# Performance work log

Measured on AMD Instinct MI355X. Metric: run time of the kernel, lower is better.

Reference implementation:

```python
import jax, jax.numpy as jnp
import numpy as np

E, T, H, I = 8, 1024, 2048, 5632  # experts, tokens/expert, hidden, intermediate


def setup_inputs() -> dict:
    key = jax.random.key(0)
    k1, k2, k3 = jax.random.split(key, 3)
    permuted_hidden_states = jax.random.normal(k1, (E * T, H), dtype=jnp.float32)
    # per-expert weights; linear is x @ W with W[in, out] (same math as nn.Linear with W^T)
    w1 = jax.random.normal(k2, (E, H, 2 * I), dtype=jnp.float32) * 0.02
    w2 = jax.random.normal(k3, (E, I, H), dtype=jnp.float32) * 0.02
    tokens_per_expert = jnp.full((E,), T, dtype=jnp.int32)
    return {
        "permuted_hidden_states": permuted_hidden_states,
        "w1": w1,
        "w2": w2,
        "tokens_per_expert": tokens_per_expert,
    }


def reference(permuted_hidden_states, w1, w2, tokens_per_expert):
    # Tokens are contiguously segmented per expert; with equal counts (static T)
    # the per-expert loop becomes one batched (grouped) GEMM.
    x = permuted_hidden_states.reshape(E, T, H)
    fc1 = jnp.einsum('eth,ehf->etf', x, w1)          # [E, T, 2I]
    a, b = jnp.split(fc1, 2, axis=-1)                # GLU: chunk last dim
    inter = jax.nn.silu(a) * b                       # [E, T, I]
    out = jnp.einsum('eti,eih->eth', inter, w2)      # [E, T, H]
    return out.reshape(E * T, H)
```

## Files before the change

kernel.cpp:

```cpp
#include <hip/hip_runtime.h>
#include <hip/hip_bf16.h>


#define EXPERTS 8
#define TOK     1024
#define HID     2048
#define INTER   5632
#define I2      (2 * INTER)

typedef __bf16 bf16x8 __attribute__((ext_vector_type(8)));
typedef float  f32x4  __attribute__((ext_vector_type(4)));

__device__ __forceinline__ unsigned short f2bf(float f) {
    union { float f; unsigned u; } v; v.f = f;
    unsigned r = v.u + 0x7FFFu + ((v.u >> 16) & 1u);
    return (unsigned short)(r >> 16);
}

__device__ __forceinline__ void gload_lds16(const void* g, void* l) {
    __builtin_amdgcn_global_load_lds(
        (const __attribute__((address_space(1))) void*)g,
        (__attribute__((address_space(3))) void*)l, 16, 0, 0);
}

__device__ __forceinline__ bf16x8 ldfrag(const unsigned short* S, int R, int kb) {
    int off = R * 64 + (kb ^ ((R & 7) << 3));
    return *reinterpret_cast<const bf16x8*>(S + off);
}


__global__ __launch_bounds__(256) void k_cvt_x(const float* __restrict__ X,
                                               unsigned short* __restrict__ Xb) {
    size_t base = ((size_t)blockIdx.x * 256 + threadIdx.x) * 8;
    int row = (int)(base >> 11);
    int k   = (int)(base & (HID - 1));
    int kp  = k ^ ((row & 7) << 3);
    float4 v0 = *reinterpret_cast<const float4*>(X + base);
    float4 v1 = *reinterpret_cast<const float4*>(X + base + 4);
    uint4 o;
    o.x = (unsigned)f2bf(v0.x) | ((unsigned)f2bf(v0.y) << 16);
    o.y = (unsigned)f2bf(v0.z) | ((unsigned)f2bf(v0.w) << 16);
    o.z = (unsigned)f2bf(v1.x) | ((unsigned)f2bf(v1.y) << 16);
    o.w = (unsigned)f2bf(v1.z) | ((unsigned)f2bf(v1.w) << 16);
    *reinterpret_cast<uint4*>(Xb + (size_t)row * HID + kp) = o;
}

__global__ __launch_bounds__(256) void k_cvt_w1(const float* __restrict__ W1,
                                                unsigned short* __restrict__ W1T) {
    __shared__ unsigned short lds[64][72];
    const int bid = blockIdx.x;
    const int hb = bid % (HID / 64);
    const int pb = (bid / (HID / 64)) % (I2 / 64);
    const int e  = bid / ((HID / 64) * (I2 / 64));
    const int h0 = hb * 64, p0 = pb * 64, n0 = p0 >> 1;
    const float* w1e = W1 + (size_t)e * HID * I2;
    const int t = threadIdx.x;
#pragma unroll
    for (int it = 0; it < 16; ++it) {
        int lin   = it * 256 + t;
        int n_off = lin & 31;
        int c     = (lin >> 5) & 1;
        int h_off = lin >> 6;
        float v = w1e[(size_t)(h0 + h_off) * I2 + c * INTER + n0 + n_off];
        lds[2 * n_off + c][h_off] = f2bf(v);
    }
    __syncthreads();
    unsigned short* o = W1T + (size_t)e * I2 * HID;
#pragma unroll
    for (int it = 0; it < 4; ++it) {
        int lin = it * 256 + t;
        int r   = lin >> 4;
        int co  = (lin & 15) * 4;
        int cop = co ^ ((r & 7) << 3);
        ushort4 v = *reinterpret_cast<ushort4*>(&lds[r][co]);
        *reinterpret_cast<ushort4*>(o + (size_t)(p0 + r) * HID + h0 + cop) = v;
    }
}

__global__ __launch_bounds__(256) void k_cvt_w2(const float* __restrict__ W2,
                                                unsigned short* __restrict__ W2T) {
    __shared__ unsigned short lds[64][72];
    const int bid = blockIdx.x;
    const int ib = bid % (INTER / 64);
    const int hb = (bid / (INTER / 64)) % (HID / 64);
    const int e  = bid / ((INTER / 64) * (HID / 64));
    const int i0 = ib * 64, h0 = hb * 64;
    const float* w2e = W2 + (size_t)e * INTER * HID;
    const int t = threadIdx.x;
#pragma unroll
    for (int it = 0; it < 16; ++it) {
        int lin   = it * 256 + t;
        int h_off = lin & 63;
        int i_off = lin >> 6;
        float v = w2e[(size_t)(i0 + i_off) * HID + h0 + h_off];
        lds[h_off][i_off] = f2bf(v);
    }
    __syncthreads();
    unsigned short* o = W2T + (size_t)e * HID * INTER;
#pragma unroll
    for (int it = 0; it < 4; ++it) {
        int lin = it * 256 + t;
        int r   = lin >> 4;
        int co  = (lin & 15) * 4;
        int cop = co ^ ((r & 7) << 3);
        ushort4 v = *reinterpret_cast<ushort4*>(&lds[r][co]);
        *reinterpret_cast<ushort4*>(o + (size_t)(h0 + r) * INTER + i0 + cop) = v;
    }
}


__device__ __forceinline__ void stage48(const unsigned short* Ab, const unsigned short* Bb,
                                        int ktot, int k0, unsigned short* buf, int t) {
#pragma unroll
    for (int j = 0; j < 4; ++j) {
        int lin = j * 512 + t;
        gload_lds16(Ab + (size_t)(lin >> 3) * ktot + k0 + (lin & 7) * 8, buf + lin * 8);
    }
#pragma unroll
    for (int j = 0; j < 2; ++j) {
        int lin = j * 512 + t;
        gload_lds16(Bb + (size_t)(lin >> 3) * ktot + k0 + (lin & 7) * 8, buf + 16384 + lin * 8);
    }
}

#define MFMA_BF16(a, b, c) __builtin_amdgcn_mfma_f32_16x16x32_bf16(a, b, c, 0, 0, 0)

__device__ __forceinline__ void gemm_ring3(const unsigned short* Ab, const unsigned short* Bb,
                                           int ktot, int nkt, f32x4 (&acc)[4][4],
                                           unsigned short* lds, int t, int lane,
                                           int wr, int wc) {
    const int cl  = lane & 15;
    const int kb0 = (lane >> 4) << 3;

    stage48(Ab, Bb, ktot, 0,  lds,         t);
    stage48(Ab, Bb, ktot, 64, lds + 24576, t);

    int c_cur = 0, c_n2 = 2;
    for (int kt = 0; kt < nkt; ++kt) {
        if (kt + 1 < nkt) { asm volatile("s_waitcnt vmcnt(6)" ::: "memory"); }
        else              { asm volatile("s_waitcnt vmcnt(0)" ::: "memory"); }
        __builtin_amdgcn_s_barrier();
        asm volatile("" ::: "memory");

        unsigned short* Ac = lds + c_cur * 24576;
        unsigned short* Bc = Ac + 16384;

        if (kt + 2 < nkt)
            stage48(Ab, Bb, ktot, (kt + 2) * 64, lds + c_n2 * 24576, t);

        bf16x8 a[2][2], b[4][2];
#pragma unroll
        for (int k = 0; k < 2; ++k)
            a[0][k] = ldfrag(Ac, wr + cl, k * 32 + kb0);
#pragma unroll
        for (int n = 0; n < 4; ++n)
#pragma unroll
            for (int k = 0; k < 2; ++k)
                b[n][k] = ldfrag(Bc, wc + n * 16 + cl, k * 32 + kb0);

#pragma unroll
        for (int m = 0; m < 4; ++m) {
            if (m < 3) {
#pragma unroll
                for (int k = 0; k < 2; ++k)
                    a[(m + 1) & 1][k] = ldfrag(Ac, wr + (m + 1) * 16 + cl, k * 32 + kb0);
            }
            __builtin_amdgcn_s_setprio(1);
#pragma unroll
            for (int n = 0; n < 4; ++n)
#pragma unroll
                for (int k = 0; k < 2; ++k)
                    acc[m][n] = MFMA_BF16(a[m & 1][k], b[n][k], acc[m][n]);
            __builtin_amdgcn_s_setprio(0);
        }

        c_cur = (c_cur == 2) ? 0 : c_cur + 1;
        c_n2  = (c_n2  == 2) ? 0 : c_n2  + 1;
    }
}

__global__ __launch_bounds__(512, 2) void k_fc1_r3(const unsigned short* __restrict__ Xb,
                                                   const unsigned short* __restrict__ W1T,
                                                   unsigned short* __restrict__ inter) {
    extern __shared__ unsigned short lds[];
    const int bid = blockIdx.x;
    const int e   = bid & 7;
    const int idx = bid >> 3;
    const int mt  = idx & 3;
    const int nt  = idx >> 2;
    const int t = threadIdx.x, lane = t & 63, w = t >> 6;
    const int wr = (w >> 1) * 64;
    const int wc = (w & 1) * 64;
    const int m0 = e * TOK + mt * 256;
    const int n0 = nt * 128;
    const unsigned short* Ab = Xb  + (size_t)m0 * HID;
    const unsigned short* Bb = W1T + (size_t)e * I2 * HID + (size_t)n0 * HID;

    f32x4 acc[4][4];
#pragma unroll
    for (int i = 0; i < 4; ++i)
#pragma unroll
        for (int j = 0; j < 4; ++j) acc[i][j] = f32x4{0.f, 0.f, 0.f, 0.f};

    gemm_ring3(Ab, Bb, HID, HID / 64, acc, lds, t, lane, wr, wc);

    const int cl = lane & 15;
    const int r0 = (lane >> 4) << 2;
#pragma unroll
    for (int mf = 0; mf < 4; ++mf)
#pragma unroll
        for (int nf = 0; nf < 4; ++nf)
#pragma unroll
            for (int r = 0; r < 4; ++r) {
                float v  = acc[mf][nf][r];
                float pv = __shfl_xor(v, 1);
                if ((lane & 1) == 0) {
                    float s = v / (1.f + __expf(-v)) * pv;
                    int row = m0 + wr + mf * 16 + r0 + r;
                    int pc  = n0 + wc + nf * 16 + cl;
                    int c   = pc >> 1;
                    int c2  = (c & ~63) | ((c & 63) ^ ((row & 7) << 3));
                    inter[(size_t)row * INTER + c2] = f2bf(s);
                }
            }
}

__global__ __launch_bounds__(512, 2) void k_fc2_r3(const unsigned short* __restrict__ A,
                                                   const unsigned short* __restrict__ W2T,
                                                   float* __restrict__ out) {
    extern __shared__ unsigned short lds[];
    const int bid = blockIdx.x;
    const int e   = bid & 7;
    const int idx = bid >> 3;
    const int mt  = idx & 3;
    const int nt  = idx >> 2;
    const int t = threadIdx.x, lane = t & 63, w = t >> 6;
    const int wr = (w >> 1) * 64;
    const int wc = (w & 1) * 64;
    const int m0 = e * TOK + mt * 256;
    const int n0 = nt * 128;
    const unsigned short* Ab = A   + (size_t)m0 * INTER;
    const unsigned short* Bb = W2T + (size_t)e * HID * INTER + (size_t)n0 * INTER;

    f32x4 acc[4][4];
#pragma unroll
    for (int i = 0; i < 4; ++i)
#pragma unroll
        for (int j = 0; j < 4; ++j) acc[i][j] = f32x4{0.f, 0.f, 0.f, 0.f};

    gemm_ring3(Ab, Bb, INTER, INTER / 64, acc, lds, t, lane, wr, wc);

    const int cl = lane & 15;
    const int r0 = (lane >> 4) << 2;
#pragma unroll
    for (int mf = 0; mf < 4; ++mf)
#pragma unroll
        for (int nf = 0; nf < 4; ++nf)
#pragma unroll
            for (int r = 0; r < 4; ++r) {
                int row = m0 + wr + mf * 16 + r0 + r;
                int col = n0 + wc + nf * 16 + cl;
                out[(size_t)row * HID + col] = acc[mf][nf][r];
            }
}


#define BM  128
#define BK  64
#define LDK 72

__global__ __launch_bounds__(256) void k_fc1_glu_fb(
    const float* __restrict__ X, const float* __restrict__ W1,
    unsigned short* __restrict__ inter)
{
    __shared__ unsigned short As[BM][LDK];
    __shared__ unsigned short Bs[128][LDK];
    const int bid = blockIdx.x;
    const int nt  = bid % (INTER / 64);
    const int mt  = (bid / (INTER / 64)) % (TOK / BM);
    const int e   = bid / ((INTER / 64) * (TOK / BM));
    const int t = threadIdx.x, lane = t & 63, w = t >> 6;
    const int m0 = mt * BM;
    const int rowbase = e * TOK + m0;
    f32x4 acc[2][8];
#pragma unroll
    for (int i = 0; i < 2; ++i)
#pragma unroll
        for (int jj = 0; jj < 8; ++jj) acc[i][jj] = f32x4{0.f, 0.f, 0.f, 0.f};
    const int jcol = t & 127;
    const int hf   = t >> 7;
    const int gcol = (jcol < 64) ? (nt * 64 + jcol) : (INTER + nt * 64 + (jcol - 64));
    const float* w1e = W1 + (size_t)e * HID * I2;
    for (int k0 = 0; k0 < HID; k0 += BK) {
#pragma unroll
        for (int it = 0; it < 8; ++it) {
            int lin = it * 256 + t;
            int r   = lin >> 4;
            int kq  = (lin & 15) << 2;
            const float4 v = *reinterpret_cast<const float4*>(
                X + (size_t)(rowbase + r) * HID + k0 + kq);
            ushort4 o;
            o.x = f2bf(v.x); o.y = f2bf(v.y); o.z = f2bf(v.z); o.w = f2bf(v.w);
            *reinterpret_cast<ushort4*>(&As[r][kq]) = o;
        }
#pragma unroll
        for (int it = 0; it < 8; ++it) {
            int kq = hf * 4 + it * 8;
            const float* p = w1e + (size_t)(k0 + kq) * I2 + gcol;
            float v0 = p[0], v1 = p[I2], v2 = p[2 * I2], v3 = p[3 * I2];
            ushort4 o;
            o.x = f2bf(v0); o.y = f2bf(v1); o.z = f2bf(v2); o.w = f2bf(v3);
            *reinterpret_cast<ushort4*>(&Bs[jcol][kq]) = o;
        }
        __syncthreads();
#pragma unroll
        for (int kk = 0; kk < 2; ++kk) {
            const int kb = kk * 32 + ((lane >> 4) << 3);
            bf16x8 a0 = *reinterpret_cast<const bf16x8*>(&As[w * 32 + (lane & 15)][kb]);
            bf16x8 a1 = *reinterpret_cast<const bf16x8*>(&As[w * 32 + 16 + (lane & 15)][kb]);
#pragma unroll
            for (int nf = 0; nf < 8; ++nf) {
                bf16x8 b = *reinterpret_cast<const bf16x8*>(&Bs[nf * 16 + (lane & 15)][kb]);
                acc[0][nf] = MFMA_BF16(a0, b, acc[0][nf]);
                acc[1][nf] = MFMA_BF16(a1, b, acc[1][nf]);
            }
        }
        __syncthreads();
    }
    const int rl0 = w * 32 + ((lane >> 4) << 2);
    const int cl  = lane & 15;
#pragma unroll
    for (int mf = 0; mf < 2; ++mf)
#pragma unroll
        for (int nfa = 0; nfa < 4; ++nfa) {
            f32x4 va = acc[mf][nfa];
            f32x4 vb = acc[mf][nfa + 4];
#pragma unroll
            for (int r = 0; r < 4; ++r) {
                float a = va[r], b = vb[r];
                float s = a / (1.f + __expf(-a)) * b;
                int row = rowbase + rl0 + mf * 16 + r;
                int col = nt * 64 + nfa * 16 + cl;
                inter[(size_t)row * INTER + col] = f2bf(s);
            }
        }
}

__global__ __launch_bounds__(256) void k_fc2_fb(
    const unsigned short* __restrict__ inter, const float* __restrict__ W2,
    float* __restrict__ out)
{
    __shared__ unsigned short As[BM][LDK];
    __shared__ unsigned short Bs[128][LDK];
    const int bid = blockIdx.x;
    const int nt  = bid % (HID / 128);
    const int mt  = (bid / (HID / 128)) % (TOK / BM);
    const int e   = bid / ((HID / 128) * (TOK / BM));
    const int t = threadIdx.x, lane = t & 63, w = t >> 6;
    const int m0 = mt * BM;
    const int rowbase = e * TOK + m0;
    f32x4 acc[2][8];
#pragma unroll
    for (int i = 0; i < 2; ++i)
#pragma unroll
        for (int jj = 0; jj < 8; ++jj) acc[i][jj] = f32x4{0.f, 0.f, 0.f, 0.f};
    const int jcol = t & 127;
    const int hf   = t >> 7;
    const int gcol = nt * 128 + jcol;
    const float* w2e = W2 + (size_t)e * INTER * HID;
    for (int k0 = 0; k0 < INTER; k0 += BK) {
#pragma unroll
        for (int it = 0; it < 4; ++it) {
            int lin = it * 256 + t;
            int r   = lin >> 3;
            int kq  = (lin & 7) << 3;
            uint4 v = *reinterpret_cast<const uint4*>(
                inter + (size_t)(rowbase + r) * INTER + k0 + kq);
            *reinterpret_cast<uint4*>(&As[r][kq]) = v;
        }
#pragma unroll
        for (int it = 0; it < 8; ++it) {
            int kq = hf * 4 + it * 8;
            const float* p = w2e + (size_t)(k0 + kq) * HID + gcol;
            float v0 = p[0], v1 = p[HID], v2 = p[2 * HID], v3 = p[3 * HID];
            ushort4 o;
            o.x = f2bf(v0); o.y = f2bf(v1); o.z = f2bf(v2); o.w = f2bf(v3);
            *reinterpret_cast<ushort4*>(&Bs[jcol][kq]) = o;
        }
        __syncthreads();
#pragma unroll
        for (int kk = 0; kk < 2; ++kk) {
            const int kb = kk * 32 + ((lane >> 4) << 3);
            bf16x8 a0 = *reinterpret_cast<const bf16x8*>(&As[w * 32 + (lane & 15)][kb]);
            bf16x8 a1 = *reinterpret_cast<const bf16x8*>(&As[w * 32 + 16 + (lane & 15)][kb]);
#pragma unroll
            for (int nf = 0; nf < 8; ++nf) {
                bf16x8 b = *reinterpret_cast<const bf16x8*>(&Bs[nf * 16 + (lane & 15)][kb]);
                acc[0][nf] = MFMA_BF16(a0, b, acc[0][nf]);
                acc[1][nf] = MFMA_BF16(a1, b, acc[1][nf]);
            }
        }
        __syncthreads();
    }
    const int rl0 = w * 32 + ((lane >> 4) << 2);
    const int cl  = lane & 15;
#pragma unroll
    for (int mf = 0; mf < 2; ++mf)
#pragma unroll
        for (int nf = 0; nf < 8; ++nf) {
            f32x4 v = acc[mf][nf];
#pragma unroll
            for (int r = 0; r < 4; ++r) {
                int row = rowbase + rl0 + mf * 16 + r;
                int col = nt * 128 + nf * 16 + cl;
                out[(size_t)row * HID + col] = v[r];
            }
        }
}


extern "C" void kernel_launch(void* const* d_in, const int* in_sizes, int n_in,
                              void* d_out, int out_size, void* d_ws, size_t ws_size,
                              hipStream_t stream) {
    const float* X  = (const float*)d_in[0];
    const float* W1 = (const float*)d_in[1];
    const float* W2 = (const float*)d_in[2];
    float* out = (float*)d_out;

    const size_t XB_B  = (size_t)EXPERTS * TOK * HID * 2;
    const size_t W1T_B = (size_t)EXPERTS * I2 * HID * 2;
    const size_t W2T_B = (size_t)EXPERTS * HID * INTER * 2;
    const size_t INT_B = (size_t)EXPERTS * TOK * INTER * 2;
    const size_t need  = XB_B + W1T_B + W2T_B + INT_B;

    if (ws_size >= need) {
        unsigned short* Xb    = (unsigned short*)d_ws;
        unsigned short* w1t   = (unsigned short*)((char*)d_ws + XB_B);
        unsigned short* w2t   = (unsigned short*)((char*)d_ws + XB_B + W1T_B);
        unsigned short* inter = (unsigned short*)((char*)d_ws + XB_B + W1T_B + W2T_B);

        hipFuncSetAttribute((const void*)k_fc1_r3,
            hipFuncAttributeMaxDynamicSharedMemorySize, 147456);
        hipFuncSetAttribute((const void*)k_fc2_r3,
            hipFuncAttributeMaxDynamicSharedMemorySize, 147456);

        dim3 b256(256), b512(512);
        k_cvt_x <<<(EXPERTS * TOK * HID) / (256 * 8), b256, 0, stream>>>(X, Xb);
        k_cvt_w1<<<EXPERTS * (I2 / 64) * (HID / 64),   b256, 0, stream>>>(W1, w1t);
        k_cvt_w2<<<EXPERTS * (HID / 64) * (INTER / 64), b256, 0, stream>>>(W2, w2t);
        k_fc1_r3<<<EXPERTS * 4 * (I2 / 128),  b512, 147456, stream>>>(Xb, w1t, inter);
        k_fc2_r3<<<EXPERTS * 4 * (HID / 128), b512, 147456, stream>>>(inter, w2t, out);
    } else {
        unsigned short* inter = (unsigned short*)d_ws;
        dim3 b256(256);
        k_fc1_glu_fb<<<EXPERTS * (TOK / BM) * (INTER / 64), b256, 0, stream>>>(X, W1, inter);
        k_fc2_fb    <<<EXPERTS * (TOK / BM) * (HID / 128),  b256, 0, stream>>>(inter, W2, out);
    }
}
```

Measured before the change: 922.6 us.

## Widen GEMM tiles to 256x256 with 1024-thread blocks and K-step 32

```diff
diff --git a/kernel.cpp b/kernel.cpp
--- a/kernel.cpp
+++ b/kernel.cpp
@@ -11,6 +11,8 @@
 typedef __bf16 bf16x8 __attribute__((ext_vector_type(8)));
 typedef float  f32x4  __attribute__((ext_vector_type(4)));
 
+#define G2(row) ((((row) >> 1) & 3) << 3)
+
 __device__ __forceinline__ unsigned short f2bf(float f) {
     union { float f; unsigned u; } v; v.f = f;
     unsigned r = v.u + 0x7FFFu + ((v.u >> 16) & 1u);
@@ -24,7 +26,7 @@
 }
 
 __device__ __forceinline__ bf16x8 ldfrag(const unsigned short* S, int R, int kb) {
-    int off = R * 64 + (kb ^ ((R & 7) << 3));
+    int off = R * 32 + (kb ^ G2(R));
     return *reinterpret_cast<const bf16x8*>(S + off);
 }
 
@@ -34,7 +36,7 @@
     size_t base = ((size_t)blockIdx.x * 256 + threadIdx.x) * 8;
     int row = (int)(base >> 11);
     int k   = (int)(base & (HID - 1));
-    int kp  = k ^ ((row & 7) << 3);
+    int kp  = k ^ G2(row);
     float4 v0 = *reinterpret_cast<const float4*>(X + base);
     float4 v1 = *reinterpret_cast<const float4*>(X + base + 4);
     uint4 o;
@@ -71,7 +73,7 @@
         int lin = it * 256 + t;
         int r   = lin >> 4;
         int co  = (lin & 15) * 4;
-        int cop = co ^ ((r & 7) << 3);
+        int cop = co ^ G2(r);
         ushort4 v = *reinterpret_cast<ushort4*>(&lds[r][co]);
         *reinterpret_cast<ushort4*>(o + (size_t)(p0 + r) * HID + h0 + cop) = v;
     }
@@ -102,25 +104,19 @@
         int lin = it * 256 + t;
         int r   = lin >> 4;
         int co  = (lin & 15) * 4;
-        int cop = co ^ ((r & 7) << 3);
+        int cop = co ^ G2(r);
         ushort4 v = *reinterpret_cast<ushort4*>(&lds[r][co]);
         *reinterpret_cast<ushort4*>(o + (size_t)(h0 + r) * INTER + i0 + cop) = v;
     }
 }
 
 
-__device__ __forceinline__ void stage48(const unsigned short* Ab, const unsigned short* Bb,
+__device__ __forceinline__ void stage32(const unsigned short* Ab, const unsigned short* Bb,
                                         int ktot, int k0, unsigned short* buf, int t) {
-#pragma unroll
-    for (int j = 0; j < 4; ++j) {
-        int lin = j * 512 + t;
-        gload_lds16(Ab + (size_t)(lin >> 3) * ktot + k0 + (lin & 7) * 8, buf + lin * 8);
-    }
-#pragma unroll
-    for (int j = 0; j < 2; ++j) {
-        int lin = j * 512 + t;
-        gload_lds16(Bb + (size_t)(lin >> 3) * ktot + k0 + (lin & 7) * 8, buf + 16384 + lin * 8);
-    }
+    const int row = t >> 2;
+    const int col = (t & 3) * 8;
+    gload_lds16(Ab + (size_t)row * ktot + k0 + col, buf + t * 8);
+    gload_lds16(Bb + (size_t)row * ktot + k0 + col, buf + 8192 + t * 8);
 }
 
 #define MFMA_BF16(a, b, c) __builtin_amdgcn_mfma_f32_16x16x32_bf16(a, b, c, 0, 0, 0)
@@ -132,45 +128,36 @@
     const int cl  = lane & 15;
     const int kb0 = (lane >> 4) << 3;
 
-    stage48(Ab, Bb, ktot, 0,  lds,         t);
-    stage48(Ab, Bb, ktot, 64, lds + 24576, t);
+    stage32(Ab, Bb, ktot, 0,  lds,         t);
+    stage32(Ab, Bb, ktot, 32, lds + 16384, t);
 
     int c_cur = 0, c_n2 = 2;
     for (int kt = 0; kt < nkt; ++kt) {
-        if (kt + 1 < nkt) { asm volatile("s_waitcnt vmcnt(6)" ::: "memory"); }
+        if (kt + 1 < nkt) { asm volatile("s_waitcnt vmcnt(2)" ::: "memory"); }
         else              { asm volatile("s_waitcnt vmcnt(0)" ::: "memory"); }
         __builtin_amdgcn_s_barrier();
         asm volatile("" ::: "memory");
 
-        unsigned short* Ac = lds + c_cur * 24576;
-        unsigned short* Bc = Ac + 16384;
+        unsigned short* Ac = lds + c_cur * 16384;
+        unsigned short* Bc = Ac + 8192;
 
         if (kt + 2 < nkt)
-            stage48(Ab, Bb, ktot, (kt + 2) * 64, lds + c_n2 * 24576, t);
-
-        bf16x8 a[2][2], b[4][2];
-#pragma unroll
-        for (int k = 0; k < 2; ++k)
-            a[0][k] = ldfrag(Ac, wr + cl, k * 32 + kb0);
+            stage32(Ab, Bb, ktot, (kt + 2) * 32, lds + c_n2 * 16384, t);
+
+        bf16x8 b[4], a[2];
 #pragma unroll
         for (int n = 0; n < 4; ++n)
-#pragma unroll
-            for (int k = 0; k < 2; ++k)
-                b[n][k] = ldfrag(Bc, wc + n * 16 + cl, k * 32 + kb0);
+            b[n] = ldfrag(Bc, wc + n * 16 + cl, kb0);
+        a[0] = ldfrag(Ac, wr + cl, kb0);
 
 #pragma unroll
         for (int m = 0; m < 4; ++m) {
-            if (m < 3) {
-#pragma unroll
-                for (int k = 0; k < 2; ++k)
-                    a[(m + 1) & 1][k] = ldfrag(Ac, wr + (m + 1) * 16 + cl, k * 32 + kb0);
-            }
+            if (m < 3)
+                a[(m + 1) & 1] = ldfrag(Ac, wr + (m + 1) * 16 + cl, kb0);
             __builtin_amdgcn_s_setprio(1);
 #pragma unroll
             for (int n = 0; n < 4; ++n)
-#pragma unroll
-                for (int k = 0; k < 2; ++k)
-                    acc[m][n] = MFMA_BF16(a[m & 1][k], b[n][k], acc[m][n]);
+                acc[m][n] = MFMA_BF16(a[m & 1], b[n], acc[m][n]);
             __builtin_amdgcn_s_setprio(0);
         }
 
@@ -179,9 +166,9 @@
     }
 }
 
-__global__ __launch_bounds__(512, 2) void k_fc1_r3(const unsigned short* __restrict__ Xb,
-                                                   const unsigned short* __restrict__ W1T,
-                                                   unsigned short* __restrict__ inter) {
+__global__ __launch_bounds__(1024, 1) void k_fc1_r3(const unsigned short* __restrict__ Xb,
+                                                    const unsigned short* __restrict__ W1T,
+                                                    unsigned short* __restrict__ inter) {
     extern __shared__ unsigned short lds[];
     const int bid = blockIdx.x;
     const int e   = bid & 7;
@@ -189,10 +176,10 @@
     const int mt  = idx & 3;
     const int nt  = idx >> 2;
     const int t = threadIdx.x, lane = t & 63, w = t >> 6;
-    const int wr = (w >> 1) * 64;
-    const int wc = (w & 1) * 64;
+    const int wr = (w >> 2) * 64;
+    const int wc = (w & 3) * 64;
     const int m0 = e * TOK + mt * 256;
-    const int n0 = nt * 128;
+    const int n0 = nt * 256;
     const unsigned short* Ab = Xb  + (size_t)m0 * HID;
     const unsigned short* Bb = W1T + (size_t)e * I2 * HID + (size_t)n0 * HID;
 
@@ -202,7 +189,7 @@
 #pragma unroll
         for (int j = 0; j < 4; ++j) acc[i][j] = f32x4{0.f, 0.f, 0.f, 0.f};
 
-    gemm_ring3(Ab, Bb, HID, HID / 64, acc, lds, t, lane, wr, wc);
+    gemm_ring3(Ab, Bb, HID, HID / 32, acc, lds, t, lane, wr, wc);
 
     const int cl = lane & 15;
     const int r0 = (lane >> 4) << 2;
@@ -219,15 +206,15 @@
                     int row = m0 + wr + mf * 16 + r0 + r;
                     int pc  = n0 + wc + nf * 16 + cl;
                     int c   = pc >> 1;
-                    int c2  = (c & ~63) | ((c & 63) ^ ((row & 7) << 3));
+                    int c2  = (c & ~31) | ((c & 31) ^ G2(row));
                     inter[(size_t)row * INTER + c2] = f2bf(s);
                 }
             }
 }
 
-__global__ __launch_bounds__(512, 2) void k_fc2_r3(const unsigned short* __restrict__ A,
-                                                   const unsigned short* __restrict__ W2T,
-                                                   float* __restrict__ out) {
+__global__ __launch_bounds__(1024, 1) void k_fc2_r3(const unsigned short* __restrict__ A,
+                                                    const unsigned short* __restrict__ W2T,
+                                                    float* __restrict__ out) {
     extern __shared__ unsigned short lds[];
     const int bid = blockIdx.x;
     const int e   = bid & 7;
@@ -235,10 +222,10 @@
     const int mt  = idx & 3;
     const int nt  = idx >> 2;
     const int t = threadIdx.x, lane = t & 63, w = t >> 6;
-    const int wr = (w >> 1) * 64;
-    const int wc = (w & 1) * 64;
+    const int wr = (w >> 2) * 64;
+    const int wc = (w & 3) * 64;
     const int m0 = e * TOK + mt * 256;
-    const int n0 = nt * 128;
+    const int n0 = nt * 256;
     const unsigned short* Ab = A   + (size_t)m0 * INTER;
     const unsigned short* Bb = W2T + (size_t)e * HID * INTER + (size_t)n0 * INTER;
 
@@ -248,7 +235,7 @@
 #pragma unroll
         for (int j = 0; j < 4; ++j) acc[i][j] = f32x4{0.f, 0.f, 0.f, 0.f};
 
-    gemm_ring3(Ab, Bb, INTER, INTER / 64, acc, lds, t, lane, wr, wc);
+    gemm_ring3(Ab, Bb, INTER, INTER / 32, acc, lds, t, lane, wr, wc);
 
     const int cl = lane & 15;
     const int r0 = (lane >> 4) << 2;
@@ -440,16 +427,16 @@
         unsigned short* inter = (unsigned short*)((char*)d_ws + XB_B + W1T_B + W2T_B);
 
         hipFuncSetAttribute((const void*)k_fc1_r3,
-            hipFuncAttributeMaxDynamicSharedMemorySize, 147456);
+            hipFuncAttributeMaxDynamicSharedMemorySize, 98304);
         hipFuncSetAttribute((const void*)k_fc2_r3,
-            hipFuncAttributeMaxDynamicSharedMemorySize, 147456);
-
-        dim3 b256(256), b512(512);
+            hipFuncAttributeMaxDynamicSharedMemorySize, 98304);
+
+        dim3 b256(256), b1024(1024);
         k_cvt_x <<<(EXPERTS * TOK * HID) / (256 * 8), b256, 0, stream>>>(X, Xb);
         k_cvt_w1<<<EXPERTS * (I2 / 64) * (HID / 64),   b256, 0, stream>>>(W1, w1t);
         k_cvt_w2<<<EXPERTS * (HID / 64) * (INTER / 64), b256, 0, stream>>>(W2, w2t);
-        k_fc1_r3<<<EXPERTS * 4 * (I2 / 128),  b512, 147456, stream>>>(Xb, w1t, inter);
-        k_fc2_r3<<<EXPERTS * 4 * (HID / 128), b512, 147456, stream>>>(inter, w2t, out);
+        k_fc1_r3<<<EXPERTS * 4 * (I2 / 256),  b1024, 98304, stream>>>(Xb, w1t, inter);
+        k_fc2_r3<<<EXPERTS * 4 * (HID / 256), b1024, 98304, stream>>>(inter, w2t, out);
     } else {
         unsigned short* inter = (unsigned short*)d_ws;
         dim3 b256(256);
```

Result: no change. 911.6 us (-1.2%).
